# Kernel tuning notes

Measured on AMD Instinct MI355X. Metric: run time of the kernel, lower is better.

Reference implementation:

```python
import jax, jax.numpy as jnp
import numpy as np

DIM = 1024
H = 8            # heads (light and heavy)
DH = 64          # dim_head
W = 64           # local attention window (light_window_size // 2)
NQ = 512         # num_heavy_tokens_q
NKV = 1024       # num_heavy_tokens_kv
EPS = 1.0        # coor descent eps
NITERS = 50      # coor descent iters
FETCH = 9.0 / 8.0
SCALE = DH ** -0.5


def _ln(x, w, b):
    m = x.mean(-1, keepdims=True)
    v = ((x - m) ** 2).mean(-1, keepdims=True)
    return (x - m) * jax.lax.rsqrt(v + 1e-5) * w + b


def _rms(x, g):
    n = jnp.maximum(jnp.linalg.norm(x, axis=-1, keepdims=True), 1e-12)
    return x / n * np.sqrt(DIM).astype(np.float32) * g


def local_attn(x, Wqkv, Wout):
    # LocalMHA, non-causal, look_backward=1, look_forward=1, window W
    b, n, _ = x.shape
    nw = n // W
    qkv = x @ Wqkv.T                      # [b,n,3*H*DH]
    q, k, v = jnp.split(qkv, 3, axis=-1)
    def towin(t):
        return t.reshape(b, nw, W, H, DH).transpose(0, 3, 1, 2, 4)  # [b,h,nw,w,dh]
    q, k, v = map(towin, (q, k, v))
    def expand(t):  # gather prev/cur/next windows -> [b,h,nw,3w,dh]
        tp = jnp.pad(t, ((0, 0), (0, 0), (1, 1), (0, 0), (0, 0)))
        return jnp.concatenate([tp[:, :, :-2], tp[:, :, 1:-1], tp[:, :, 2:]], axis=3)
    ke, ve = expand(k), expand(v)
    sim = jnp.einsum('bhnid,bhnjd->bhnij', q, ke) * SCALE
    win = jnp.arange(nw)
    valid = jnp.concatenate([
        jnp.repeat((win > 0)[:, None], W, 1),
        jnp.ones((nw, W), bool),
        jnp.repeat((win < nw - 1)[:, None], W, 1)], axis=1)  # [nw,3w]
    sim = jnp.where(valid[None, None, :, None, :], sim, -1e9)
    attn = jax.nn.softmax(sim, axis=-1)
    o = jnp.einsum('bhnij,bhnjd->bhnid', attn, ve)
    o = o.transpose(0, 2, 3, 1, 4).reshape(b, n, H * DH)
    return o @ Wout.T


def route(x, routing_token, num_tokens):
    # CoordinateDescentRouter with num_routing_tokens=1, straight_through=True
    s = jnp.einsum('bnd,rd->brn', x, routing_token).reshape(x.shape[0], x.shape[1])
    n = s.shape[-1]
    logk = jnp.log(jnp.asarray(min(num_tokens * FETCH, float(n)), s.dtype))
    def body(ab, _):
        a, bb = ab
        a = EPS * (logk - jax.nn.logsumexp((s + bb) / EPS, axis=-1, keepdims=True))
        bb = -jax.nn.relu(s + a)
        return (a, bb), None
    (a, bb), _ = jax.lax.scan(body, (jnp.zeros((s.shape[0], 1), s.dtype), -s), None, length=NITERS)
    scores = jnp.exp((s + a + bb) / EPS)
    sel_scores, sel_idx = jax.lax.top_k(scores, num_tokens)
    # straight-through: forward value 1.0, gradient of identity
    sel_scores = sel_scores + jax.lax.stop_gradient(1.0 - sel_scores)
    return sel_scores, sel_idx


def heavy_attn(xq, ctx, scores_kv, gamma, Wq, Wkv, Wout, null_kv):
    b = xq.shape[0]
    xq = _rms(xq, gamma)
    ctx = _rms(ctx, gamma)
    q = (xq @ Wq.T).reshape(b, -1, H, DH).transpose(0, 2, 1, 3)           # [b,h,nq,dh]
    kv = (ctx @ Wkv.T).reshape(b, -1, H, 2 * DH).transpose(0, 2, 1, 3)    # [b,h,nkv,2dh]
    k, v = kv[..., :DH], kv[..., DH:]
    v = v * scores_kv[:, None, :, None]
    nk = jnp.broadcast_to(null_kv[0][None, :, None, :], (b, H, 1, DH))
    nv = jnp.broadcast_to(null_kv[1][None, :, None, :], (b, H, 1, DH))
    k = jnp.concatenate([nk, k], axis=2)
    v = jnp.concatenate([nv, v], axis=2)
    sim = jnp.einsum('bhid,bhjd->bhij', q, k) * SCALE
    attn = jax.nn.softmax(sim, axis=-1)
    o = jnp.einsum('bhij,bhjd->bhid', attn, v)
    o = o.transpose(0, 2, 1, 3).reshape(b, -1, H * DH)
    return o @ Wout.T


def setup_inputs() -> dict:
    key = jax.random.key(0)
    ks = jax.random.split(key, 12)
    D, IN = DIM, H * DH
    w = lambda k, shape: jax.random.normal(k, shape, jnp.float32) * 0.02
    return {
        'x': jax.random.normal(ks[0], (4, 4096, D), jnp.float32),
        'ln_w': jnp.ones((D,), jnp.float32),
        'ln_b': jnp.zeros((D,), jnp.float32),
        'Wqkv': w(ks[1], (3 * IN, D)),
        'Wout_l': w(ks[2], (D, IN)),
        'rt_q': jax.random.normal(ks[3], (1, D), jnp.float32),
        'rt_kv': jax.random.normal(ks[4], (1, D), jnp.float32),
        'gamma': jnp.ones((D,), jnp.float32),
        'Wq': w(ks[5], (IN, D)),
        'Wkv': w(ks[6], (2 * IN, D)),
        'Wout_h': w(ks[7], (D, IN)),
        'null_kv': jax.random.normal(ks[8], (2, H, DH), jnp.float32),
        'null_q': jax.random.normal(ks[9], (D,), jnp.float32),
    }


def reference(x, ln_w, ln_b, Wqkv, Wout_l, rt_q, rt_kv, gamma, Wq, Wkv, Wout_h, null_kv, null_q):
    b, n, d = x.shape
    light = local_attn(_ln(x, ln_w, ln_b), Wqkv, Wout_l)
    sq, iq = route(x, rt_q, NQ)
    skv, ikv = route(x, rt_kv, NKV)
    br = jnp.arange(b)[:, None]
    xq = x[br, iq]          # gather routed queries  [b,NQ,d]
    xkv = x[br, ikv]        # gather routed kv       [b,NKV,d]
    heavy = heavy_attn(xq, xkv, skv, gamma, Wq, Wkv, Wout_h, null_kv)
    heavy = heavy * sq[..., None]
    out = jnp.broadcast_to(null_q[None, None, :], (b, n, d))
    out = out.at[br, iq].set(heavy)   # scatter heavy branch back
    return out + light
```

## Files before the change

kernel.cpp:

```cpp
#include <hip/hip_runtime.h>
#include <hip/hip_bf16.h>

typedef __attribute__((ext_vector_type(8))) short bv8;
typedef __attribute__((ext_vector_type(4))) float fv4;
typedef __hip_bfloat16 bf16;

#define MFMA16(a,b,c) __builtin_amdgcn_mfma_f32_16x16x32_bf16((a),(b),(c),0,0,0)
#define GLOAD_LDS(gp, lp) __builtin_amdgcn_global_load_lds( \
    (const __attribute__((address_space(1))) void*)(gp), \
    (__attribute__((address_space(3))) void*)(lp), 16, 0, 0)

template<int NW>
__device__ __forceinline__ float blockReduceSumF(float v) {
  #pragma unroll
  for (int m = 1; m < 64; m <<= 1) v += __shfl_xor(v, m, 64);
  __shared__ float sm[NW];
  if ((threadIdx.x & 63) == 0) sm[threadIdx.x >> 6] = v;
  __syncthreads();
  float t = 0.f;
  #pragma unroll
  for (int i = 0; i < NW; ++i) t += sm[i];
  __syncthreads();
  return t;
}

template<int NW>
__device__ __forceinline__ double blockReduceMaxD(double v) {
  #pragma unroll
  for (int m = 1; m < 64; m <<= 1) v = fmax(v, __shfl_xor(v, m, 64));
  __shared__ double sm[NW];
  if ((threadIdx.x & 63) == 0) sm[threadIdx.x >> 6] = v;
  __syncthreads();
  double t = sm[0];
  #pragma unroll
  for (int i = 1; i < NW; ++i) t = fmax(t, sm[i]);
  __syncthreads();
  return t;
}

__global__ __launch_bounds__(256)
void cast5_kernel(const float* __restrict__ a0, const float* __restrict__ a1,
                  const float* __restrict__ a2, const float* __restrict__ a3,
                  const float* __restrict__ a4,
                  bf16* __restrict__ b0, bf16* __restrict__ b1, bf16* __restrict__ b2,
                  bf16* __restrict__ b3, bf16* __restrict__ b4) {
  size_t g = ((size_t)blockIdx.x * 256 + threadIdx.x) * 8;
  const float* src; bf16* dst; size_t off;
  if (g < 1572864)      { src = a0; dst = b0; off = g; }
  else if (g < 2097152) { src = a1; dst = b1; off = g - 1572864; }
  else if (g < 2621440) { src = a2; dst = b2; off = g - 2097152; }
  else if (g < 3670016) { src = a3; dst = b3; off = g - 2621440; }
  else                  { src = a4; dst = b4; off = g - 3670016; }
  float4 v0 = *(const float4*)(src + off);
  float4 v1 = *(const float4*)(src + off + 4);
  bv8 o;
  ((bf16*)&o)[0] = __float2bfloat16(v0.x); ((bf16*)&o)[1] = __float2bfloat16(v0.y);
  ((bf16*)&o)[2] = __float2bfloat16(v0.z); ((bf16*)&o)[3] = __float2bfloat16(v0.w);
  ((bf16*)&o)[4] = __float2bfloat16(v1.x); ((bf16*)&o)[5] = __float2bfloat16(v1.y);
  ((bf16*)&o)[6] = __float2bfloat16(v1.z); ((bf16*)&o)[7] = __float2bfloat16(v1.w);
  *(bv8*)(dst + off) = o;
}

__global__ __launch_bounds__(256)
void ln_sdot_kernel(const float* __restrict__ x, const float* __restrict__ w,
                    const float* __restrict__ bb, const float* __restrict__ rtq,
                    const float* __restrict__ rtkv, bf16* __restrict__ out,
                    double* __restrict__ s) {
  const int r = blockIdx.x;
  const float* xr = x + (size_t)r * 1024;
  float v4[4]; float ssum = 0.f;
  double dq = 0.0, dk = 0.0;
  #pragma unroll
  for (int i = 0; i < 4; ++i) {
    int d = threadIdx.x + i * 256;
    float v = xr[d];
    v4[i] = v; ssum += v;
    dq += (double)v * (double)rtq[d];
    dk += (double)v * (double)rtkv[d];
  }
  ssum = blockReduceSumF<4>(ssum);
  const float mean = ssum * (1.0f / 1024.0f);
  float vs = 0.f;
  #pragma unroll
  for (int i = 0; i < 4; ++i) { float d = v4[i] - mean; vs += d * d; }
  vs = blockReduceSumF<4>(vs);
  const float rstd = 1.0f / sqrtf(vs * (1.0f / 1024.0f) + 1e-5f);
  #pragma unroll
  for (int m = 1; m < 64; m <<= 1) { dq += __shfl_xor(dq, m, 64); dk += __shfl_xor(dk, m, 64); }
  __shared__ double smq[4], smk[4];
  if ((threadIdx.x & 63) == 0) { smq[threadIdx.x >> 6] = dq; smk[threadIdx.x >> 6] = dk; }
  __syncthreads();
  if (threadIdx.x == 0) {
    s[r] = smq[0] + smq[1] + smq[2] + smq[3];
    s[16384 + r] = smk[0] + smk[1] + smk[2] + smk[3];
  }
  bf16* orow = out + (size_t)r * 1024;
  #pragma unroll
  for (int i = 0; i < 4; ++i) {
    int d = threadIdx.x + i * 256;
    orow[d] = __float2bfloat16((v4[i] - mean) * rstd * w[d] + bb[d]);
  }
}

__global__ __launch_bounds__(256, 1)
void route_sel_kernel(const double* __restrict__ s_all, int* __restrict__ iq,
                      int* __restrict__ ikv, int* __restrict__ posq) {
  const int route = blockIdx.x >> 2, b = blockIdx.x & 3;
  const double* s = s_all + route * 16384 + b * 4096;
  const double K = (route == 0) ? 576.0 : 1152.0;
  const int KSEL = (route == 0) ? 512 : 1024;
  const int tid = threadIdx.x;
  const int lane = tid & 63, wid = tid >> 6;
  __shared__ double evbuf[4096];
  __shared__ double a_sh;
  __shared__ int scn[256];

  double sv[16];
  #pragma unroll
  for (int i = 0; i < 16; ++i) sv[i] = s[tid * 16 + i];
  double mx = sv[0];
  #pragma unroll
  for (int i = 1; i < 16; ++i) mx = fmax(mx, sv[i]);
  mx = blockReduceMaxD<4>(mx);
  #pragma unroll
  for (int i = 0; i < 16; ++i) evbuf[tid * 16 + i] = exp(sv[i] - mx);
  __syncthreads();

  if (wid == 0) {
    double e64[64];
    #pragma unroll
    for (int j = 0; j < 64; ++j) e64[j] = evbuf[j * 64 + lane];
    double z = (4096.0 / K) * exp(-mx);
    for (int it = 1; it < 50; ++it) {
      double a0 = 0.0, a1 = 0.0, a2 = 0.0, a3 = 0.0;
      #pragma unroll
      for (int j = 0; j < 64; j += 4) {
        a0 += fmin(e64[j], z);
        a1 += fmin(e64[j + 1], z);
        a2 += fmin(e64[j + 2], z);
        a3 += fmin(e64[j + 3], z);
      }
      double t = (a0 + a1) + (a2 + a3);
      #pragma unroll
      for (int m = 1; m < 64; m <<= 1) t += __shfl_xor(t, m, 64);
      z = t / K;
    }
    if (lane == 0) a_sh = -mx - log(z);
  }
  __syncthreads();
  const double a = a_sh;

  float scf[16]; int m16 = 0;
  #pragma unroll
  for (int i = 0; i < 16; ++i) {
    scf[i] = (float)exp(fmin(sv[i] + a, 0.0));
    m16 += (scf[i] == 1.0f) ? 1 : 0;
  }
  scn[tid] = m16;
  __syncthreads();
  for (int off = 1; off < 256; off <<= 1) {
    int v = (tid >= off) ? scn[tid - off] : 0;
    __syncthreads();
    scn[tid] += v;
    __syncthreads();
  }
  const int total = scn[255];
  const int excl = scn[tid] - m16;
  if (total >= KSEL) {
    int rk = excl;
    #pragma unroll
    for (int i = 0; i < 16; ++i) {
      if (scf[i] == 1.0f) {
        if (rk < KSEL) {
          int idx = tid * 16 + i;
          if (route == 0) { iq[b * 512 + rk] = idx; posq[b * 4096 + idx] = rk; }
          else            { ikv[b * 1024 + rk] = idx; }
        }
        rk++;
      }
    }
  } else {
    unsigned long long* keys = (unsigned long long*)evbuf;
    #pragma unroll
    for (int i = 0; i < 16; ++i) {
      unsigned bits = __float_as_uint(scf[i]);
      keys[tid * 16 + i] = ((unsigned long long)(~bits) << 32) | (unsigned long long)(tid * 16 + i);
    }
    for (int k = 2; k <= 4096; k <<= 1) {
      for (int j = k >> 1; j > 0; j >>= 1) {
        __syncthreads();
        for (int t = tid; t < 2048; t += 256) {
          int i2 = ((t & ~(j - 1)) << 1) | (t & (j - 1));
          int ip = i2 + j;
          unsigned long long av = keys[i2], bvv = keys[ip];
          bool up = ((i2 & k) == 0);
          if (up ? (av > bvv) : (av < bvv)) { keys[i2] = bvv; keys[ip] = av; }
        }
      }
    }
    __syncthreads();
    for (int j2 = tid; j2 < KSEL; j2 += 256) {
      int idx = (int)(keys[j2] & 0xFFFFFFFFull);
      if (route == 0) { iq[b * 512 + j2] = idx; posq[b * 4096 + idx] = j2; }
      else            { ikv[b * 1024 + j2] = idx; }
    }
  }
}

__global__ __launch_bounds__(256)
void gather_rms_kernel(const float* __restrict__ x, const float* __restrict__ gamma,
                       const int* __restrict__ iq, const int* __restrict__ ikv,
                       bf16* __restrict__ xq, bf16* __restrict__ xkv) {
  const int bid = blockIdx.x;
  const float* src; bf16* dst;
  if (bid < 2048) {
    int b = bid >> 9, j = bid & 511;
    int tok = iq[b * 512 + j];
    src = x + ((size_t)(b * 4096 + tok)) * 1024;
    dst = xq + (size_t)bid * 1024;
  } else {
    int id = bid - 2048;
    int b = id >> 10, j = id & 1023;
    int tok = ikv[b * 1024 + j];
    src = x + ((size_t)(b * 4096 + tok)) * 1024;
    dst = xkv + (size_t)id * 1024;
  }
  float v4[4]; float ss = 0.f;
  #pragma unroll
  for (int i = 0; i < 4; ++i) { v4[i] = src[threadIdx.x + i * 256]; ss += v4[i] * v4[i]; }
  ss = blockReduceSumF<4>(ss);
  const float nrm = fmaxf(sqrtf(ss), 1e-12f);
  const float scl = 32.0f / nrm;
  #pragma unroll
  for (int i = 0; i < 4; ++i) {
    int d = threadIdx.x + i * 256;
    dst[d] = __float2bfloat16(v4[i] * scl * gamma[d]);
  }
}

template<int EPI>
__global__ __launch_bounds__(256)
void gemm_bt(const bf16* __restrict__ A, const bf16* __restrict__ B, void* __restrict__ Cout,
             int M, int N, int K,
             const int* __restrict__ posq, const float* __restrict__ heavy,
             const float* __restrict__ nullq) {
  __shared__ alignas(16) bf16 As[128 * 32];
  __shared__ alignas(16) bf16 Bs[128 * 32];
  const int tid = threadIdx.x;
  const int lane = tid & 63, w = tid >> 6;
  const int wr = w >> 1, wc = w & 1;
  const int lrow = lane & 15, lk = (lane >> 4) * 8;
  const int d = blockIdx.y * gridDim.x + blockIdx.x;
  const int q = d >> 3;
  const int col = q % gridDim.x;
  const int panel = (d & 7) + 8 * (q / gridDim.x);
  const int row0 = panel * 128, col0 = col * 128;
  fv4 acc[4][4];
  #pragma unroll
  for (int m = 0; m < 4; ++m)
    #pragma unroll
    for (int n = 0; n < 4; ++n) acc[m][n] = (fv4){0.f, 0.f, 0.f, 0.f};
  const int ob0 = w * 2048;
  for (int k0 = 0; k0 < K; k0 += 32) {
    #pragma unroll
    for (int t = 0; t < 2; ++t) {
      int ob = ob0 + t * 1024;
      int ofl = ob + lane * 16;
      int r = ofl >> 6, c8 = ((ofl >> 4) & 3) * 8;
      GLOAD_LDS(A + (size_t)(row0 + r) * K + k0 + c8, (char*)As + ob);
      GLOAD_LDS(B + (size_t)(col0 + r) * K + k0 + c8, (char*)Bs + ob);
    }
    __syncthreads();
    bv8 af[4], bfr[4];
    #pragma unroll
    for (int m = 0; m < 4; ++m) af[m] = *(bv8*)&As[(wr * 64 + m * 16 + lrow) * 32 + lk];
    #pragma unroll
    for (int n = 0; n < 4; ++n) bfr[n] = *(bv8*)&Bs[(wc * 64 + n * 16 + lrow) * 32 + lk];
    #pragma unroll
    for (int m = 0; m < 4; ++m)
      #pragma unroll
      for (int n = 0; n < 4; ++n)
        acc[m][n] = MFMA16(af[m], bfr[n], acc[m][n]);
    __syncthreads();
  }
  #pragma unroll
  for (int m = 0; m < 4; ++m) {
    int gr0 = row0 + wr * 64 + m * 16 + (lane >> 4) * 4;
    #pragma unroll
    for (int n = 0; n < 4; ++n) {
      int gc = col0 + wc * 64 + n * 16 + lrow;
      #pragma unroll
      for (int r = 0; r < 4; ++r) {
        int grow = gr0 + r;
        float vv = acc[m][n][r];
        if (EPI == 0) {
          ((bf16*)Cout)[(size_t)grow * N + gc] = __float2bfloat16(vv);
        } else if (EPI == 1) {
          ((float*)Cout)[(size_t)grow * N + gc] = vv;
        } else {
          int p = posq[grow];
          float add = (p >= 0) ? heavy[((size_t)((grow >> 12) * 512 + p)) * 1024 + gc]
                               : nullq[gc];
          ((float*)Cout)[(size_t)grow * N + gc] = vv + add;
        }
      }
    }
  }
}

__global__ __launch_bounds__(256)
void local_attn_kernel(const bf16* __restrict__ qkv, bf16* __restrict__ olight) {
  const int w = blockIdx.x, h = blockIdx.y, b = blockIdx.z;
  const int tid = threadIdx.x;
  const int lane = tid & 63, wv = tid >> 6;
  const int lrow = lane & 15, lkg = lane >> 4;
  __shared__ bf16 Qs[64][72], Ks[64][72], Vts[64][72], Ps[64][72];
  {
    const size_t baseq = ((size_t)(b * 4096 + w * 64)) * 1536 + h * 64;
    #pragma unroll
    for (int v = 0; v < 2; ++v) {
      int vec = tid + v * 256; int i = vec >> 3, dd = (vec & 7) * 8;
      *(bv8*)&Qs[i][dd] = *(const bv8*)&qkv[baseq + (size_t)i * 1536 + dd];
    }
  }
  fv4 oacc[4];
  float m_run[4], l_run[4];
  #pragma unroll
  for (int n = 0; n < 4; ++n) oacc[n] = (fv4){0.f, 0.f, 0.f, 0.f};
  #pragma unroll
  for (int r = 0; r < 4; ++r) { m_run[r] = -INFINITY; l_run[r] = 0.f; }
  for (int c = 0; c < 3; ++c) {
    int sw = w - 1 + c;
    if (sw < 0 || sw >= 64) continue;
    __syncthreads();
    const size_t bkv = ((size_t)(b * 4096 + sw * 64)) * 1536 + h * 64;
    #pragma unroll
    for (int v = 0; v < 2; ++v) {
      int vec = tid + v * 256; int i = vec >> 3, dd = (vec & 7) * 8;
      *(bv8*)&Ks[i][dd] = *(const bv8*)&qkv[bkv + 512 + (size_t)i * 1536 + dd];
    }
    #pragma unroll
    for (int v = 0; v < 2; ++v) {
      int vec = tid + v * 256; int j = vec >> 3, d0 = (vec & 7) * 8;
      bv8 val = *(const bv8*)&qkv[bkv + 1024 + (size_t)j * 1536 + d0];
      #pragma unroll
      for (int i = 0; i < 8; ++i) Vts[d0 + i][j] = ((bf16*)&val)[i];
    }
    __syncthreads();
    fv4 sa[4];
    #pragma unroll
    for (int n = 0; n < 4; ++n) {
      sa[n] = (fv4){0.f, 0.f, 0.f, 0.f};
      #pragma unroll
      for (int ks = 0; ks < 2; ++ks) {
        bv8 aq = *(bv8*)&Qs[wv * 16 + lrow][lkg * 8 + ks * 32];
        bv8 bk = *(bv8*)&Ks[n * 16 + lrow][lkg * 8 + ks * 32];
        sa[n] = MFMA16(aq, bk, sa[n]);
      }
    }
    float mc[4];
    #pragma unroll
    for (int r = 0; r < 4; ++r) {
      #pragma unroll
      for (int n = 0; n < 4; ++n) sa[n][r] *= 0.125f;
      mc[r] = fmaxf(fmaxf(sa[0][r], sa[1][r]), fmaxf(sa[2][r], sa[3][r]));
    }
    #pragma unroll
    for (int m = 1; m < 16; m <<= 1)
      #pragma unroll
      for (int r = 0; r < 4; ++r) mc[r] = fmaxf(mc[r], __shfl_xor(mc[r], m, 64));
    float p[4][4], ls[4];
    #pragma unroll
    for (int r = 0; r < 4; ++r) {
      float mn = fmaxf(m_run[r], mc[r]);
      float scl = expf(m_run[r] - mn);
      ls[r] = 0.f;
      #pragma unroll
      for (int n = 0; n < 4; ++n) { p[n][r] = expf(sa[n][r] - mn); ls[r] += p[n][r]; }
      m_run[r] = mn;
      l_run[r] *= scl;
      #pragma unroll
      for (int n = 0; n < 4; ++n) oacc[n][r] *= scl;
    }
    #pragma unroll
    for (int m = 1; m < 16; m <<= 1)
      #pragma unroll
      for (int r = 0; r < 4; ++r) ls[r] += __shfl_xor(ls[r], m, 64);
    #pragma unroll
    for (int r = 0; r < 4; ++r) l_run[r] += ls[r];
    #pragma unroll
    for (int n = 0; n < 4; ++n)
      #pragma unroll
      for (int r = 0; r < 4; ++r)
        Ps[wv * 16 + lkg * 4 + r][n * 16 + lrow] = __float2bfloat16(p[n][r]);
    __syncthreads();
    #pragma unroll
    for (int n = 0; n < 4; ++n)
      #pragma unroll
      for (int ks = 0; ks < 2; ++ks) {
        bv8 ap = *(bv8*)&Ps[wv * 16 + lrow][lkg * 8 + ks * 32];
        bv8 bvv = *(bv8*)&Vts[n * 16 + lrow][lkg * 8 + ks * 32];
        oacc[n] = MFMA16(ap, bvv, oacc[n]);
      }
  }
  const size_t ob = ((size_t)(b * 4096 + w * 64 + wv * 16)) * 512 + h * 64;
  #pragma unroll
  for (int n = 0; n < 4; ++n)
    #pragma unroll
    for (int r = 0; r < 4; ++r) {
      int row = lkg * 4 + r;
      olight[ob + (size_t)row * 512 + n * 16 + lrow] = __float2bfloat16(oacc[n][r] / l_run[r]);
    }
}

__global__ __launch_bounds__(256)
void heavy_attn_split_kernel(const bf16* __restrict__ qh, const bf16* __restrict__ kvh,
                             const float* __restrict__ nkv, float* __restrict__ o_part,
                             float* __restrict__ ml_part) {
  const int qt = blockIdx.x, h = blockIdx.y;
  const int b = blockIdx.z >> 2, s = blockIdx.z & 3;
  const int tid = threadIdx.x;
  const int lane = tid & 63, wv = tid >> 6;
  const int lrow = lane & 15, lkg = lane >> 4;
  __shared__ bf16 Qs[64][72], Ks[64][72], Vts[64][72], Ps[64][72];
  {
    const size_t baseq = ((size_t)(b * 512 + qt * 64)) * 512 + h * 64;
    #pragma unroll
    for (int v = 0; v < 2; ++v) {
      int vec = tid + v * 256; int i = vec >> 3, dd = (vec & 7) * 8;
      *(bv8*)&Qs[i][dd] = *(const bv8*)&qh[baseq + (size_t)i * 512 + dd];
    }
  }
  fv4 oacc[4];
  float m_run[4], l_run[4];
  #pragma unroll
  for (int n = 0; n < 4; ++n) oacc[n] = (fv4){0.f, 0.f, 0.f, 0.f};
  #pragma unroll
  for (int r = 0; r < 4; ++r) { m_run[r] = -INFINITY; l_run[r] = 0.f; }
  const int cs = (s == 0) ? 0 : (s * 4 + 1);
  const int ce = s * 4 + 5;
  for (int c = cs; c < ce; ++c) {
    __syncthreads();
    #pragma unroll
    for (int v = 0; v < 2; ++v) {
      int vec = tid + v * 256; int j = vec >> 3, dd = (vec & 7) * 8;
      int kvg = c * 64 + j;
      bv8 val;
      if (kvg >= 1 && kvg <= 1024) {
        val = *(const bv8*)&kvh[((size_t)(b * 1024 + kvg - 1)) * 1024 + h * 128 + dd];
      } else if (kvg == 0) {
        #pragma unroll
        for (int t = 0; t < 8; ++t) ((bf16*)&val)[t] = __float2bfloat16(nkv[h * 64 + dd + t]);
      } else {
        #pragma unroll
        for (int t = 0; t < 8; ++t) ((short*)&val)[t] = 0;
      }
      *(bv8*)&Ks[j][dd] = val;
    }
    #pragma unroll
    for (int v = 0; v < 2; ++v) {
      int vec = tid + v * 256; int j = vec >> 3, d0 = (vec & 7) * 8;
      int kvg = c * 64 + j;
      if (kvg >= 1 && kvg <= 1024) {
        bv8 val = *(const bv8*)&kvh[((size_t)(b * 1024 + kvg - 1)) * 1024 + h * 128 + 64 + d0];
        #pragma unroll
        for (int i = 0; i < 8; ++i) Vts[d0 + i][j] = ((bf16*)&val)[i];
      } else if (kvg == 0) {
        #pragma unroll
        for (int i = 0; i < 8; ++i) Vts[d0 + i][j] = __float2bfloat16(nkv[512 + h * 64 + d0 + i]);
      } else {
        #pragma unroll
        for (int i = 0; i < 8; ++i) Vts[d0 + i][j] = __float2bfloat16(0.0f);
      }
    }
    __syncthreads();
    fv4 sa[4];
    #pragma unroll
    for (int n = 0; n < 4; ++n) {
      sa[n] = (fv4){0.f, 0.f, 0.f, 0.f};
      #pragma unroll
      for (int ks = 0; ks < 2; ++ks) {
        bv8 aq = *(bv8*)&Qs[wv * 16 + lrow][lkg * 8 + ks * 32];
        bv8 bk = *(bv8*)&Ks[n * 16 + lrow][lkg * 8 + ks * 32];
        sa[n] = MFMA16(aq, bk, sa[n]);
      }
    }
    float mc[4];
    #pragma unroll
    for (int r = 0; r < 4; ++r) {
      #pragma unroll
      for (int n = 0; n < 4; ++n) {
        sa[n][r] *= 0.125f;
        int kvg = c * 64 + n * 16 + lrow;
        if (kvg > 1024) sa[n][r] = -1e30f;
      }
      mc[r] = fmaxf(fmaxf(sa[0][r], sa[1][r]), fmaxf(sa[2][r], sa[3][r]));
    }
    #pragma unroll
    for (int m = 1; m < 16; m <<= 1)
      #pragma unroll
      for (int r = 0; r < 4; ++r) mc[r] = fmaxf(mc[r], __shfl_xor(mc[r], m, 64));
    float p[4][4], ls[4];
    #pragma unroll
    for (int r = 0; r < 4; ++r) {
      float mn = fmaxf(m_run[r], mc[r]);
      float scl = expf(m_run[r] - mn);
      ls[r] = 0.f;
      #pragma unroll
      for (int n = 0; n < 4; ++n) { p[n][r] = expf(sa[n][r] - mn); ls[r] += p[n][r]; }
      m_run[r] = mn;
      l_run[r] *= scl;
      #pragma unroll
      for (int n = 0; n < 4; ++n) oacc[n][r] *= scl;
    }
    #pragma unroll
    for (int m = 1; m < 16; m <<= 1)
      #pragma unroll
      for (int r = 0; r < 4; ++r) ls[r] += __shfl_xor(ls[r], m, 64);
    #pragma unroll
    for (int r = 0; r < 4; ++r) l_run[r] += ls[r];
    #pragma unroll
    for (int n = 0; n < 4; ++n)
      #pragma unroll
      for (int r = 0; r < 4; ++r)
        Ps[wv * 16 + lkg * 4 + r][n * 16 + lrow] = __float2bfloat16(p[n][r]);
    __syncthreads();
    #pragma unroll
    for (int n = 0; n < 4; ++n)
      #pragma unroll
      for (int ks = 0; ks < 2; ++ks) {
        bv8 ap = *(bv8*)&Ps[wv * 16 + lrow][lkg * 8 + ks * 32];
        bv8 bvv = *(bv8*)&Vts[n * 16 + lrow][lkg * 8 + ks * 32];
        oacc[n] = MFMA16(ap, bvv, oacc[n]);
      }
  }
  const int idx = (((s * 4 + b) * 8 + h) * 8 + qt);
  float* ob = o_part + (size_t)idx * 4096;
  #pragma unroll
  for (int n = 0; n < 4; ++n)
    #pragma unroll
    for (int r = 0; r < 4; ++r) {
      int row = wv * 16 + lkg * 4 + r;
      ob[row * 64 + n * 16 + lrow] = oacc[n][r];
    }
  if (lrow == 0) {
    #pragma unroll
    for (int r = 0; r < 4; ++r) {
      int row = wv * 16 + lkg * 4 + r;
      ml_part[idx * 128 + row] = m_run[r];
      ml_part[idx * 128 + 64 + row] = l_run[r];
    }
  }
}

__global__ __launch_bounds__(256)
void heavy_combine_kernel(const float* __restrict__ o_part, const float* __restrict__ ml_part,
                          bf16* __restrict__ oh) {
  const int qt = blockIdx.x, h = blockIdx.y, b = blockIdx.z;
  const int tid = threadIdx.x;
  const int row = tid >> 2, c0 = (tid & 3) * 16;
  int idx[4]; float m[4], l[4];
  #pragma unroll
  for (int s = 0; s < 4; ++s) {
    idx[s] = (((s * 4 + b) * 8 + h) * 8 + qt);
    m[s] = ml_part[idx[s] * 128 + row];
    l[s] = ml_part[idx[s] * 128 + 64 + row];
  }
  const float mstar = fmaxf(fmaxf(m[0], m[1]), fmaxf(m[2], m[3]));
  float wsum = 0.f, w[4];
  #pragma unroll
  for (int s = 0; s < 4; ++s) { w[s] = expf(m[s] - mstar); wsum += w[s] * l[s]; }
  const float inv = 1.0f / wsum;
  float o[16];
  #pragma unroll
  for (int i = 0; i < 16; ++i) o[i] = 0.f;
  #pragma unroll
  for (int s = 0; s < 4; ++s) {
    const fv4* op = (const fv4*)(o_part + (size_t)idx[s] * 4096 + row * 64 + c0);
    #pragma unroll
    for (int k = 0; k < 4; ++k) {
      fv4 v = op[k];
      #pragma unroll
      for (int j = 0; j < 4; ++j) o[k * 4 + j] += w[s] * v[j];
    }
  }
  const size_t ob = ((size_t)(b * 512 + qt * 64 + row)) * 512 + h * 64 + c0;
  bv8 pk[2];
  #pragma unroll
  for (int i = 0; i < 16; ++i) ((bf16*)pk)[i] = __float2bfloat16(o[i] * inv);
  *(bv8*)&oh[ob] = pk[0];
  *(bv8*)&oh[ob + 8] = pk[1];
}

extern "C" void kernel_launch(void* const* d_in, const int* in_sizes, int n_in,
                              void* d_out, int out_size, void* d_ws, size_t ws_size,
                              hipStream_t stream) {
  (void)in_sizes; (void)n_in; (void)out_size; (void)ws_size;
  const float* x     = (const float*)d_in[0];
  const float* ln_w  = (const float*)d_in[1];
  const float* ln_b  = (const float*)d_in[2];
  const float* Wqkv  = (const float*)d_in[3];
  const float* Woutl = (const float*)d_in[4];
  const float* rtq   = (const float*)d_in[5];
  const float* rtkv  = (const float*)d_in[6];
  const float* gamma = (const float*)d_in[7];
  const float* Wq    = (const float*)d_in[8];
  const float* Wkv   = (const float*)d_in[9];
  const float* Wouth = (const float*)d_in[10];
  const float* nkv   = (const float*)d_in[11];
  const float* nq    = (const float*)d_in[12];
  float* out = (float*)d_out;

  char* ws = (char*)d_ws;
  size_t off = 0;
  auto alloc = [&](size_t bytes) -> void* {
    void* p = ws + off;
    off = (off + bytes + 255) & ~(size_t)255;
    return p;
  };
  bf16* ln_bf    = (bf16*)alloc(16384ull * 1024 * 2);
  bf16* qkv_bf   = (bf16*)alloc(16384ull * 1536 * 2);
  bf16* ol_bf    = (bf16*)alloc(16384ull * 512 * 2);
  bf16* Wqkv_bf  = (bf16*)alloc(1536ull * 1024 * 2);
  bf16* Woutl_bf = (bf16*)alloc(1024ull * 512 * 2);
  bf16* Wq_bf    = (bf16*)alloc(512ull * 1024 * 2);
  bf16* Wkv_bf   = (bf16*)alloc(1024ull * 1024 * 2);
  bf16* Wouth_bf = (bf16*)alloc(1024ull * 512 * 2);
  double* s_d    = (double*)alloc(32768ull * 8);
  int* iq        = (int*)alloc(2048ull * 4);
  int* ikv       = (int*)alloc(4096ull * 4);
  int* posq      = (int*)alloc(16384ull * 4);
  bf16* xq_bf    = (bf16*)alloc(2048ull * 1024 * 2);
  bf16* xkv_bf   = (bf16*)alloc(4096ull * 1024 * 2);
  bf16* qh_bf    = (bf16*)alloc(2048ull * 512 * 2);
  bf16* kvh_bf   = (bf16*)alloc(4096ull * 1024 * 2);
  bf16* oh_bf    = (bf16*)alloc(2048ull * 512 * 2);
  float* heavy_f = (float*)alloc(2048ull * 1024 * 4);
  float* o_part  = (float*)alloc(4096ull * 4096 * 4);
  float* ml_part = (float*)alloc(4096ull * 128 * 4);

  cast5_kernel<<<2048, 256, 0, stream>>>(Wqkv, Woutl, Wq, Wkv, Wouth,
                                         Wqkv_bf, Woutl_bf, Wq_bf, Wkv_bf, Wouth_bf);

  ln_sdot_kernel<<<16384, 256, 0, stream>>>(x, ln_w, ln_b, rtq, rtkv, ln_bf, s_d);

  hipMemsetAsync(posq, 0xFF, 16384 * 4, stream);
  route_sel_kernel<<<8, 256, 0, stream>>>(s_d, iq, ikv, posq);

  gemm_bt<0><<<dim3(12, 128), 256, 0, stream>>>(ln_bf, Wqkv_bf, qkv_bf, 16384, 1536, 1024,
                                                nullptr, nullptr, nullptr);
  local_attn_kernel<<<dim3(64, 8, 4), 256, 0, stream>>>(qkv_bf, ol_bf);

  gather_rms_kernel<<<6144, 256, 0, stream>>>(x, gamma, iq, ikv, xq_bf, xkv_bf);
  gemm_bt<0><<<dim3(4, 16), 256, 0, stream>>>(xq_bf, Wq_bf, qh_bf, 2048, 512, 1024,
                                              nullptr, nullptr, nullptr);
  gemm_bt<0><<<dim3(8, 32), 256, 0, stream>>>(xkv_bf, Wkv_bf, kvh_bf, 4096, 1024, 1024,
                                              nullptr, nullptr, nullptr);
  heavy_attn_split_kernel<<<dim3(8, 8, 16), 256, 0, stream>>>(qh_bf, kvh_bf, nkv, o_part, ml_part);
  heavy_combine_kernel<<<dim3(8, 8, 4), 256, 0, stream>>>(o_part, ml_part, oh_bf);
  gemm_bt<1><<<dim3(8, 16), 256, 0, stream>>>(oh_bf, Wouth_bf, heavy_f, 2048, 1024, 512,
                                              nullptr, nullptr, nullptr);

  gemm_bt<2><<<dim3(8, 128), 256, 0, stream>>>(ol_bf, Woutl_bf, out, 16384, 1024, 512,
                                               posq, heavy_f, nq);
}
```

Measured before the change: 326.7 us.

## Merge independent kernels into combined launches and store split partials in bf16

Several launches are merged into single kernels that branch on block index. The weight cast, LayerNorm/routing-dot and posq memset become one prep kernel. Local attention and the routed gather+RMSNorm share one launch, and the Wq and Wkv projection GEMMs share another, which cuts launch gaps and lets small kernels fill the GPU together. Split-KV heavy attention partial outputs are also stored as bf16 instead of fp32, halving that traffic at some cost in precision.

```diff
diff --git a/kernel.cpp b/kernel.cpp
--- a/kernel.cpp
+++ b/kernel.cpp
@@ -39,66 +39,71 @@
 }
 
 __global__ __launch_bounds__(256)
-void cast5_kernel(const float* __restrict__ a0, const float* __restrict__ a1,
-                  const float* __restrict__ a2, const float* __restrict__ a3,
-                  const float* __restrict__ a4,
-                  bf16* __restrict__ b0, bf16* __restrict__ b1, bf16* __restrict__ b2,
-                  bf16* __restrict__ b3, bf16* __restrict__ b4) {
-  size_t g = ((size_t)blockIdx.x * 256 + threadIdx.x) * 8;
-  const float* src; bf16* dst; size_t off;
-  if (g < 1572864)      { src = a0; dst = b0; off = g; }
-  else if (g < 2097152) { src = a1; dst = b1; off = g - 1572864; }
-  else if (g < 2621440) { src = a2; dst = b2; off = g - 2097152; }
-  else if (g < 3670016) { src = a3; dst = b3; off = g - 2621440; }
-  else                  { src = a4; dst = b4; off = g - 3670016; }
-  float4 v0 = *(const float4*)(src + off);
-  float4 v1 = *(const float4*)(src + off + 4);
-  bv8 o;
-  ((bf16*)&o)[0] = __float2bfloat16(v0.x); ((bf16*)&o)[1] = __float2bfloat16(v0.y);
-  ((bf16*)&o)[2] = __float2bfloat16(v0.z); ((bf16*)&o)[3] = __float2bfloat16(v0.w);
-  ((bf16*)&o)[4] = __float2bfloat16(v1.x); ((bf16*)&o)[5] = __float2bfloat16(v1.y);
-  ((bf16*)&o)[6] = __float2bfloat16(v1.z); ((bf16*)&o)[7] = __float2bfloat16(v1.w);
-  *(bv8*)(dst + off) = o;
-}
-
-__global__ __launch_bounds__(256)
-void ln_sdot_kernel(const float* __restrict__ x, const float* __restrict__ w,
-                    const float* __restrict__ bb, const float* __restrict__ rtq,
-                    const float* __restrict__ rtkv, bf16* __restrict__ out,
-                    double* __restrict__ s) {
-  const int r = blockIdx.x;
-  const float* xr = x + (size_t)r * 1024;
-  float v4[4]; float ssum = 0.f;
-  double dq = 0.0, dk = 0.0;
-  #pragma unroll
-  for (int i = 0; i < 4; ++i) {
-    int d = threadIdx.x + i * 256;
-    float v = xr[d];
-    v4[i] = v; ssum += v;
-    dq += (double)v * (double)rtq[d];
-    dk += (double)v * (double)rtkv[d];
-  }
-  ssum = blockReduceSumF<4>(ssum);
-  const float mean = ssum * (1.0f / 1024.0f);
-  float vs = 0.f;
-  #pragma unroll
-  for (int i = 0; i < 4; ++i) { float d = v4[i] - mean; vs += d * d; }
-  vs = blockReduceSumF<4>(vs);
-  const float rstd = 1.0f / sqrtf(vs * (1.0f / 1024.0f) + 1e-5f);
-  #pragma unroll
-  for (int m = 1; m < 64; m <<= 1) { dq += __shfl_xor(dq, m, 64); dk += __shfl_xor(dk, m, 64); }
-  __shared__ double smq[4], smk[4];
-  if ((threadIdx.x & 63) == 0) { smq[threadIdx.x >> 6] = dq; smk[threadIdx.x >> 6] = dk; }
-  __syncthreads();
-  if (threadIdx.x == 0) {
-    s[r] = smq[0] + smq[1] + smq[2] + smq[3];
-    s[16384 + r] = smk[0] + smk[1] + smk[2] + smk[3];
-  }
-  bf16* orow = out + (size_t)r * 1024;
-  #pragma unroll
-  for (int i = 0; i < 4; ++i) {
-    int d = threadIdx.x + i * 256;
-    orow[d] = __float2bfloat16((v4[i] - mean) * rstd * w[d] + bb[d]);
+void prep_kernel(const float* __restrict__ x, const float* __restrict__ lnw,
+                 const float* __restrict__ lnb, const float* __restrict__ rtq,
+                 const float* __restrict__ rtkv, bf16* __restrict__ lnout,
+                 double* __restrict__ s,
+                 const float* __restrict__ a0, const float* __restrict__ a1,
+                 const float* __restrict__ a2, const float* __restrict__ a3,
+                 const float* __restrict__ a4,
+                 bf16* __restrict__ b0, bf16* __restrict__ b1, bf16* __restrict__ b2,
+                 bf16* __restrict__ b3, bf16* __restrict__ b4,
+                 int* __restrict__ posq) {
+  const int bid = blockIdx.x;
+  if (bid < 16384) {
+    const int r = bid;
+    const float* xr = x + (size_t)r * 1024;
+    float v4[4]; float ssum = 0.f;
+    double dq = 0.0, dk = 0.0;
+    #pragma unroll
+    for (int i = 0; i < 4; ++i) {
+      int d = threadIdx.x + i * 256;
+      float v = xr[d];
+      v4[i] = v; ssum += v;
+      dq += (double)v * (double)rtq[d];
+      dk += (double)v * (double)rtkv[d];
+    }
+    ssum = blockReduceSumF<4>(ssum);
+    const float mean = ssum * (1.0f / 1024.0f);
+    float vs = 0.f;
+    #pragma unroll
+    for (int i = 0; i < 4; ++i) { float d = v4[i] - mean; vs += d * d; }
+    vs = blockReduceSumF<4>(vs);
+    const float rstd = 1.0f / sqrtf(vs * (1.0f / 1024.0f) + 1e-5f);
+    #pragma unroll
+    for (int m = 1; m < 64; m <<= 1) { dq += __shfl_xor(dq, m, 64); dk += __shfl_xor(dk, m, 64); }
+    __shared__ double smq[4], smk[4];
+    if ((threadIdx.x & 63) == 0) { smq[threadIdx.x >> 6] = dq; smk[threadIdx.x >> 6] = dk; }
+    __syncthreads();
+    if (threadIdx.x == 0) {
+      s[r] = smq[0] + smq[1] + smq[2] + smq[3];
+      s[16384 + r] = smk[0] + smk[1] + smk[2] + smk[3];
+    }
+    bf16* orow = lnout + (size_t)r * 1024;
+    #pragma unroll
+    for (int i = 0; i < 4; ++i) {
+      int d = threadIdx.x + i * 256;
+      orow[d] = __float2bfloat16((v4[i] - mean) * rstd * lnw[d] + lnb[d]);
+    }
+  } else if (bid < 18432) {
+    size_t g = ((size_t)(bid - 16384) * 256 + threadIdx.x) * 8;
+    const float* src; bf16* dst; size_t off;
+    if (g < 1572864)      { src = a0; dst = b0; off = g; }
+    else if (g < 2097152) { src = a1; dst = b1; off = g - 1572864; }
+    else if (g < 2621440) { src = a2; dst = b2; off = g - 2097152; }
+    else if (g < 3670016) { src = a3; dst = b3; off = g - 2621440; }
+    else                  { src = a4; dst = b4; off = g - 3670016; }
+    float4 v0 = *(const float4*)(src + off);
+    float4 v1 = *(const float4*)(src + off + 4);
+    bv8 o;
+    ((bf16*)&o)[0] = __float2bfloat16(v0.x); ((bf16*)&o)[1] = __float2bfloat16(v0.y);
+    ((bf16*)&o)[2] = __float2bfloat16(v0.z); ((bf16*)&o)[3] = __float2bfloat16(v0.w);
+    ((bf16*)&o)[4] = __float2bfloat16(v1.x); ((bf16*)&o)[5] = __float2bfloat16(v1.y);
+    ((bf16*)&o)[6] = __float2bfloat16(v1.z); ((bf16*)&o)[7] = __float2bfloat16(v1.w);
+    *(bv8*)(dst + off) = o;
+  } else {
+    int i0 = (bid - 18432) * 1024 + threadIdx.x * 4;
+    posq[i0] = -1; posq[i0 + 1] = -1; posq[i0 + 2] = -1; posq[i0 + 3] = -1;
   }
 }
 
@@ -207,54 +212,16 @@
   }
 }
 
-__global__ __launch_bounds__(256)
-void gather_rms_kernel(const float* __restrict__ x, const float* __restrict__ gamma,
-                       const int* __restrict__ iq, const int* __restrict__ ikv,
-                       bf16* __restrict__ xq, bf16* __restrict__ xkv) {
-  const int bid = blockIdx.x;
-  const float* src; bf16* dst;
-  if (bid < 2048) {
-    int b = bid >> 9, j = bid & 511;
-    int tok = iq[b * 512 + j];
-    src = x + ((size_t)(b * 4096 + tok)) * 1024;
-    dst = xq + (size_t)bid * 1024;
-  } else {
-    int id = bid - 2048;
-    int b = id >> 10, j = id & 1023;
-    int tok = ikv[b * 1024 + j];
-    src = x + ((size_t)(b * 4096 + tok)) * 1024;
-    dst = xkv + (size_t)id * 1024;
-  }
-  float v4[4]; float ss = 0.f;
-  #pragma unroll
-  for (int i = 0; i < 4; ++i) { v4[i] = src[threadIdx.x + i * 256]; ss += v4[i] * v4[i]; }
-  ss = blockReduceSumF<4>(ss);
-  const float nrm = fmaxf(sqrtf(ss), 1e-12f);
-  const float scl = 32.0f / nrm;
-  #pragma unroll
-  for (int i = 0; i < 4; ++i) {
-    int d = threadIdx.x + i * 256;
-    dst[d] = __float2bfloat16(v4[i] * scl * gamma[d]);
-  }
-}
-
 template<int EPI>
-__global__ __launch_bounds__(256)
-void gemm_bt(const bf16* __restrict__ A, const bf16* __restrict__ B, void* __restrict__ Cout,
-             int M, int N, int K,
-             const int* __restrict__ posq, const float* __restrict__ heavy,
-             const float* __restrict__ nullq) {
-  __shared__ alignas(16) bf16 As[128 * 32];
-  __shared__ alignas(16) bf16 Bs[128 * 32];
+__device__ __forceinline__ void gemm_core(
+    const bf16* __restrict__ A, const bf16* __restrict__ B, void* __restrict__ Cout,
+    int N, int K, int row0, int col0, bf16* As, bf16* Bs,
+    const int* __restrict__ posq, const float* __restrict__ heavy,
+    const float* __restrict__ nullq) {
   const int tid = threadIdx.x;
   const int lane = tid & 63, w = tid >> 6;
   const int wr = w >> 1, wc = w & 1;
   const int lrow = lane & 15, lk = (lane >> 4) * 8;
-  const int d = blockIdx.y * gridDim.x + blockIdx.x;
-  const int q = d >> 3;
-  const int col = q % gridDim.x;
-  const int panel = (d & 7) + 8 * (q / gridDim.x);
-  const int row0 = panel * 128, col0 = col * 128;
   fv4 acc[4][4];
   #pragma unroll
   for (int m = 0; m < 4; ++m)
@@ -308,114 +275,182 @@
   }
 }
 
+__device__ __forceinline__ void xcd_remap(int d, int gx, int& row0, int& col0) {
+  int q = d >> 3;
+  col0 = (q % gx) * 128;
+  row0 = ((d & 7) + 8 * (q / gx)) * 128;
+}
+
+template<int EPI>
 __global__ __launch_bounds__(256)
-void local_attn_kernel(const bf16* __restrict__ qkv, bf16* __restrict__ olight) {
-  const int w = blockIdx.x, h = blockIdx.y, b = blockIdx.z;
+void gemm_bt(const bf16* __restrict__ A, const bf16* __restrict__ B, void* __restrict__ Cout,
+             int N, int K,
+             const int* __restrict__ posq, const float* __restrict__ heavy,
+             const float* __restrict__ nullq) {
+  __shared__ alignas(16) bf16 As[128 * 32];
+  __shared__ alignas(16) bf16 Bs[128 * 32];
+  int row0, col0;
+  xcd_remap(blockIdx.y * gridDim.x + blockIdx.x, gridDim.x, row0, col0);
+  gemm_core<EPI>(A, B, Cout, N, K, row0, col0, As, Bs, posq, heavy, nullq);
+}
+
+__global__ __launch_bounds__(256)
+void wqkv_gemm_kernel(const bf16* __restrict__ xkv, const bf16* __restrict__ Wkv,
+                      bf16* __restrict__ kvh,
+                      const bf16* __restrict__ xq, const bf16* __restrict__ Wq,
+                      bf16* __restrict__ qh) {
+  __shared__ alignas(16) bf16 As[128 * 32];
+  __shared__ alignas(16) bf16 Bs[128 * 32];
+  const int bid = blockIdx.x;
+  int row0, col0;
+  if (bid < 256) {
+    xcd_remap(bid, 8, row0, col0);
+    gemm_core<0>(xkv, Wkv, kvh, 1024, 1024, row0, col0, As, Bs, nullptr, nullptr, nullptr);
+  } else {
+    xcd_remap(bid - 256, 4, row0, col0);
+    gemm_core<0>(xq, Wq, qh, 512, 1024, row0, col0, As, Bs, nullptr, nullptr, nullptr);
+  }
+}
+
+__global__ __launch_bounds__(256)
+void la_gather_kernel(const bf16* __restrict__ qkv, bf16* __restrict__ olight,
+                      const float* __restrict__ x, const float* __restrict__ gamma,
+                      const int* __restrict__ iq, const int* __restrict__ ikv,
+                      bf16* __restrict__ xq, bf16* __restrict__ xkv) {
+  __shared__ bf16 Qs[64][72], Ks[64][72], Vts[64][72], Ps[64][72];
   const int tid = threadIdx.x;
-  const int lane = tid & 63, wv = tid >> 6;
-  const int lrow = lane & 15, lkg = lane >> 4;
-  __shared__ bf16 Qs[64][72], Ks[64][72], Vts[64][72], Ps[64][72];
-  {
-    const size_t baseq = ((size_t)(b * 4096 + w * 64)) * 1536 + h * 64;
-    #pragma unroll
-    for (int v = 0; v < 2; ++v) {
-      int vec = tid + v * 256; int i = vec >> 3, dd = (vec & 7) * 8;
-      *(bv8*)&Qs[i][dd] = *(const bv8*)&qkv[baseq + (size_t)i * 1536 + dd];
-    }
-  }
-  fv4 oacc[4];
-  float m_run[4], l_run[4];
-  #pragma unroll
-  for (int n = 0; n < 4; ++n) oacc[n] = (fv4){0.f, 0.f, 0.f, 0.f};
-  #pragma unroll
-  for (int r = 0; r < 4; ++r) { m_run[r] = -INFINITY; l_run[r] = 0.f; }
-  for (int c = 0; c < 3; ++c) {
-    int sw = w - 1 + c;
-    if (sw < 0 || sw >= 64) continue;
-    __syncthreads();
-    const size_t bkv = ((size_t)(b * 4096 + sw * 64)) * 1536 + h * 64;
-    #pragma unroll
-    for (int v = 0; v < 2; ++v) {
-      int vec = tid + v * 256; int i = vec >> 3, dd = (vec & 7) * 8;
-      *(bv8*)&Ks[i][dd] = *(const bv8*)&qkv[bkv + 512 + (size_t)i * 1536 + dd];
-    }
-    #pragma unroll
-    for (int v = 0; v < 2; ++v) {
-      int vec = tid + v * 256; int j = vec >> 3, d0 = (vec & 7) * 8;
-      bv8 val = *(const bv8*)&qkv[bkv + 1024 + (size_t)j * 1536 + d0];
-      #pragma unroll
-      for (int i = 0; i < 8; ++i) Vts[d0 + i][j] = ((bf16*)&val)[i];
-    }
-    __syncthreads();
-    fv4 sa[4];
-    #pragma unroll
-    for (int n = 0; n < 4; ++n) {
-      sa[n] = (fv4){0.f, 0.f, 0.f, 0.f};
-      #pragma unroll
-      for (int ks = 0; ks < 2; ++ks) {
-        bv8 aq = *(bv8*)&Qs[wv * 16 + lrow][lkg * 8 + ks * 32];
-        bv8 bk = *(bv8*)&Ks[n * 16 + lrow][lkg * 8 + ks * 32];
-        sa[n] = MFMA16(aq, bk, sa[n]);
-      }
-    }
-    float mc[4];
-    #pragma unroll
-    for (int r = 0; r < 4; ++r) {
-      #pragma unroll
-      for (int n = 0; n < 4; ++n) sa[n][r] *= 0.125f;
-      mc[r] = fmaxf(fmaxf(sa[0][r], sa[1][r]), fmaxf(sa[2][r], sa[3][r]));
-    }
-    #pragma unroll
-    for (int m = 1; m < 16; m <<= 1)
-      #pragma unroll
-      for (int r = 0; r < 4; ++r) mc[r] = fmaxf(mc[r], __shfl_xor(mc[r], m, 64));
-    float p[4][4], ls[4];
-    #pragma unroll
-    for (int r = 0; r < 4; ++r) {
-      float mn = fmaxf(m_run[r], mc[r]);
-      float scl = expf(m_run[r] - mn);
-      ls[r] = 0.f;
-      #pragma unroll
-      for (int n = 0; n < 4; ++n) { p[n][r] = expf(sa[n][r] - mn); ls[r] += p[n][r]; }
-      m_run[r] = mn;
-      l_run[r] *= scl;
-      #pragma unroll
-      for (int n = 0; n < 4; ++n) oacc[n][r] *= scl;
-    }
-    #pragma unroll
-    for (int m = 1; m < 16; m <<= 1)
-      #pragma unroll
-      for (int r = 0; r < 4; ++r) ls[r] += __shfl_xor(ls[r], m, 64);
-    #pragma unroll
-    for (int r = 0; r < 4; ++r) l_run[r] += ls[r];
+  if (blockIdx.x < 2048) {
+    const int w = blockIdx.x & 63, h = (blockIdx.x >> 6) & 7, b = blockIdx.x >> 9;
+    const int lane = tid & 63, wv = tid >> 6;
+    const int lrow = lane & 15, lkg = lane >> 4;
+    {
+      const size_t baseq = ((size_t)(b * 4096 + w * 64)) * 1536 + h * 64;
+      #pragma unroll
+      for (int v = 0; v < 2; ++v) {
+        int vec = tid + v * 256; int i = vec >> 3, dd = (vec & 7) * 8;
+        *(bv8*)&Qs[i][dd] = *(const bv8*)&qkv[baseq + (size_t)i * 1536 + dd];
+      }
+    }
+    fv4 oacc[4];
+    float m_run[4], l_run[4];
+    #pragma unroll
+    for (int n = 0; n < 4; ++n) oacc[n] = (fv4){0.f, 0.f, 0.f, 0.f};
+    #pragma unroll
+    for (int r = 0; r < 4; ++r) { m_run[r] = -INFINITY; l_run[r] = 0.f; }
+    for (int c = 0; c < 3; ++c) {
+      int sw = w - 1 + c;
+      if (sw < 0 || sw >= 64) continue;
+      __syncthreads();
+      const size_t bkv = ((size_t)(b * 4096 + sw * 64)) * 1536 + h * 64;
+      #pragma unroll
+      for (int v = 0; v < 2; ++v) {
+        int vec = tid + v * 256; int i = vec >> 3, dd = (vec & 7) * 8;
+        *(bv8*)&Ks[i][dd] = *(const bv8*)&qkv[bkv + 512 + (size_t)i * 1536 + dd];
+      }
+      #pragma unroll
+      for (int v = 0; v < 2; ++v) {
+        int vec = tid + v * 256; int j = vec >> 3, d0 = (vec & 7) * 8;
+        bv8 val = *(const bv8*)&qkv[bkv + 1024 + (size_t)j * 1536 + d0];
+        #pragma unroll
+        for (int i = 0; i < 8; ++i) Vts[d0 + i][j] = ((bf16*)&val)[i];
+      }
+      __syncthreads();
+      fv4 sa[4];
+      #pragma unroll
+      for (int n = 0; n < 4; ++n) {
+        sa[n] = (fv4){0.f, 0.f, 0.f, 0.f};
+        #pragma unroll
+        for (int ks = 0; ks < 2; ++ks) {
+          bv8 aq = *(bv8*)&Qs[wv * 16 + lrow][lkg * 8 + ks * 32];
+          bv8 bk = *(bv8*)&Ks[n * 16 + lrow][lkg * 8 + ks * 32];
+          sa[n] = MFMA16(aq, bk, sa[n]);
+        }
+      }
+      float mc[4];
+      #pragma unroll
+      for (int r = 0; r < 4; ++r) {
+        #pragma unroll
+        for (int n = 0; n < 4; ++n) sa[n][r] *= 0.125f;
+        mc[r] = fmaxf(fmaxf(sa[0][r], sa[1][r]), fmaxf(sa[2][r], sa[3][r]));
+      }
+      #pragma unroll
+      for (int m = 1; m < 16; m <<= 1)
+        #pragma unroll
+        for (int r = 0; r < 4; ++r) mc[r] = fmaxf(mc[r], __shfl_xor(mc[r], m, 64));
+      float p[4][4], ls[4];
+      #pragma unroll
+      for (int r = 0; r < 4; ++r) {
+        float mn = fmaxf(m_run[r], mc[r]);
+        float scl = expf(m_run[r] - mn);
+        ls[r] = 0.f;
+        #pragma unroll
+        for (int n = 0; n < 4; ++n) { p[n][r] = expf(sa[n][r] - mn); ls[r] += p[n][r]; }
+        m_run[r] = mn;
+        l_run[r] *= scl;
+        #pragma unroll
+        for (int n = 0; n < 4; ++n) oacc[n][r] *= scl;
+      }
+      #pragma unroll
+      for (int m = 1; m < 16; m <<= 1)
+        #pragma unroll
+        for (int r = 0; r < 4; ++r) ls[r] += __shfl_xor(ls[r], m, 64);
+      #pragma unroll
+      for (int r = 0; r < 4; ++r) l_run[r] += ls[r];
+      #pragma unroll
+      for (int n = 0; n < 4; ++n)
+        #pragma unroll
+        for (int r = 0; r < 4; ++r)
+          Ps[wv * 16 + lkg * 4 + r][n * 16 + lrow] = __float2bfloat16(p[n][r]);
+      __syncthreads();
+      #pragma unroll
+      for (int n = 0; n < 4; ++n)
+        #pragma unroll
+        for (int ks = 0; ks < 2; ++ks) {
+          bv8 ap = *(bv8*)&Ps[wv * 16 + lrow][lkg * 8 + ks * 32];
+          bv8 bvv = *(bv8*)&Vts[n * 16 + lrow][lkg * 8 + ks * 32];
+          oacc[n] = MFMA16(ap, bvv, oacc[n]);
+        }
+    }
+    const size_t ob = ((size_t)(b * 4096 + w * 64 + wv * 16)) * 512 + h * 64;
     #pragma unroll
     for (int n = 0; n < 4; ++n)
       #pragma unroll
-      for (int r = 0; r < 4; ++r)
-        Ps[wv * 16 + lkg * 4 + r][n * 16 + lrow] = __float2bfloat16(p[n][r]);
-    __syncthreads();
-    #pragma unroll
-    for (int n = 0; n < 4; ++n)
-      #pragma unroll
-      for (int ks = 0; ks < 2; ++ks) {
-        bv8 ap = *(bv8*)&Ps[wv * 16 + lrow][lkg * 8 + ks * 32];
-        bv8 bvv = *(bv8*)&Vts[n * 16 + lrow][lkg * 8 + ks * 32];
-        oacc[n] = MFMA16(ap, bvv, oacc[n]);
-      }
-  }
-  const size_t ob = ((size_t)(b * 4096 + w * 64 + wv * 16)) * 512 + h * 64;
-  #pragma unroll
-  for (int n = 0; n < 4; ++n)
-    #pragma unroll
-    for (int r = 0; r < 4; ++r) {
-      int row = lkg * 4 + r;
-      olight[ob + (size_t)row * 512 + n * 16 + lrow] = __float2bfloat16(oacc[n][r] / l_run[r]);
-    }
+      for (int r = 0; r < 4; ++r) {
+        int row = lkg * 4 + r;
+        olight[ob + (size_t)row * 512 + n * 16 + lrow] = __float2bfloat16(oacc[n][r] / l_run[r]);
+      }
+  } else {
+    const int bid = blockIdx.x - 2048;
+    const float* src; bf16* dst;
+    if (bid < 2048) {
+      int b = bid >> 9, j = bid & 511;
+      int tok = iq[b * 512 + j];
+      src = x + ((size_t)(b * 4096 + tok)) * 1024;
+      dst = xq + (size_t)bid * 1024;
+    } else {
+      int id = bid - 2048;
+      int b = id >> 10, j = id & 1023;
+      int tok = ikv[b * 1024 + j];
+      src = x + ((size_t)(b * 4096 + tok)) * 1024;
+      dst = xkv + (size_t)id * 1024;
+    }
+    float v4[4]; float ss = 0.f;
+    #pragma unroll
+    for (int i = 0; i < 4; ++i) { v4[i] = src[tid + i * 256]; ss += v4[i] * v4[i]; }
+    ss = blockReduceSumF<4>(ss);
+    const float nrm = fmaxf(sqrtf(ss), 1e-12f);
+    const float scl = 32.0f / nrm;
+    #pragma unroll
+    for (int i = 0; i < 4; ++i) {
+      int d = tid + i * 256;
+      dst[d] = __float2bfloat16(v4[i] * scl * gamma[d]);
+    }
+  }
 }
 
 __global__ __launch_bounds__(256)
 void heavy_attn_split_kernel(const bf16* __restrict__ qh, const bf16* __restrict__ kvh,
-                             const float* __restrict__ nkv, float* __restrict__ o_part,
+                             const float* __restrict__ nkv, bf16* __restrict__ o_part,
                              float* __restrict__ ml_part) {
   const int qt = blockIdx.x, h = blockIdx.y;
   const int b = blockIdx.z >> 2, s = blockIdx.z & 3;
@@ -535,13 +570,13 @@
       }
   }
   const int idx = (((s * 4 + b) * 8 + h) * 8 + qt);
-  float* ob = o_part + (size_t)idx * 4096;
+  bf16* ob = o_part + (size_t)idx * 4096;
   #pragma unroll
   for (int n = 0; n < 4; ++n)
     #pragma unroll
     for (int r = 0; r < 4; ++r) {
       int row = wv * 16 + lkg * 4 + r;
-      ob[row * 64 + n * 16 + lrow] = oacc[n][r];
+      ob[row * 64 + n * 16 + lrow] = __float2bfloat16(oacc[n][r]);
     }
   if (lrow == 0) {
     #pragma unroll
@@ -554,7 +589,7 @@
 }
 
 __global__ __launch_bounds__(256)
-void heavy_combine_kernel(const float* __restrict__ o_part, const float* __restrict__ ml_part,
+void heavy_combine_kernel(const bf16* __restrict__ o_part, const float* __restrict__ ml_part,
                           bf16* __restrict__ oh) {
   const int qt = blockIdx.x, h = blockIdx.y, b = blockIdx.z;
   const int tid = threadIdx.x;
@@ -576,13 +611,13 @@
   for (int i = 0; i < 16; ++i) o[i] = 0.f;
   #pragma unroll
   for (int s = 0; s < 4; ++s) {
-    const fv4* op = (const fv4*)(o_part + (size_t)idx[s] * 4096 + row * 64 + c0);
-    #pragma unroll
-    for (int k = 0; k < 4; ++k) {
-      fv4 v = op[k];
-      #pragma unroll
-      for (int j = 0; j < 4; ++j) o[k * 4 + j] += w[s] * v[j];
-    }
+    const bf16* op = o_part + (size_t)idx[s] * 4096 + row * 64 + c0;
+    bv8 v0 = *(const bv8*)op;
+    bv8 v1 = *(const bv8*)(op + 8);
+    #pragma unroll
+    for (int j = 0; j < 8; ++j) o[j] += w[s] * __bfloat162float(((bf16*)&v0)[j]);
+    #pragma unroll
+    for (int j = 0; j < 8; ++j) o[8 + j] += w[s] * __bfloat162float(((bf16*)&v1)[j]);
   }
   const size_t ob = ((size_t)(b * 512 + qt * 64 + row)) * 512 + h * 64 + c0;
   bv8 pk[2];
@@ -636,31 +671,28 @@
   bf16* kvh_bf   = (bf16*)alloc(4096ull * 1024 * 2);
   bf16* oh_bf    = (bf16*)alloc(2048ull * 512 * 2);
   float* heavy_f = (float*)alloc(2048ull * 1024 * 4);
-  float* o_part  = (float*)alloc(4096ull * 4096 * 4);
+  bf16* o_part   = (bf16*)alloc(4096ull * 4096 * 2);
   float* ml_part = (float*)alloc(4096ull * 128 * 4);
 
-  cast5_kernel<<<2048, 256, 0, stream>>>(Wqkv, Woutl, Wq, Wkv, Wouth,
-                                         Wqkv_bf, Woutl_bf, Wq_bf, Wkv_bf, Wouth_bf);
-
-  ln_sdot_kernel<<<16384, 256, 0, stream>>>(x, ln_w, ln_b, rtq, rtkv, ln_bf, s_d);
-
-  hipMemsetAsync(posq, 0xFF, 16384 * 4, stream);
+  prep_kernel<<<18448, 256, 0, stream>>>(x, ln_w, ln_b, rtq, rtkv, ln_bf, s_d,
+                                         Wqkv, Woutl, Wq, Wkv, Wouth,
+                                         Wqkv_bf, Woutl_bf, Wq_bf, Wkv_bf, Wouth_bf,
+                                         posq);
+
   route_sel_kernel<<<8, 256, 0, stream>>>(s_d, iq, ikv, posq);
 
-  gemm_bt<0><<<dim3(12, 128), 256, 0, stream>>>(ln_bf, Wqkv_bf, qkv_bf, 16384, 1536, 1024,
+  gemm_bt<0><<<dim3(12, 128), 256, 0, stream>>>(ln_bf, Wqkv_bf, qkv_bf, 1536, 1024,
                                                 nullptr, nullptr, nullptr);
-  local_attn_kernel<<<dim3(64, 8, 4), 256, 0, stream>>>(qkv_bf, ol_bf);
-
-  gather_rms_kernel<<<6144, 256, 0, stream>>>(x, gamma, iq, ikv, xq_bf, xkv_bf);
-  gemm_bt<0><<<dim3(4, 16), 256, 0, stream>>>(xq_bf, Wq_bf, qh_bf, 2048, 512, 1024,
-                                              nullptr, nullptr, nullptr);
-  gemm_bt<0><<<dim3(8, 32), 256, 0, stream>>>(xkv_bf, Wkv_bf, kvh_bf, 4096, 1024, 1024,
-                                              nullptr, nullptr, nullptr);
+
+  la_gather_kernel<<<8192, 256, 0, stream>>>(qkv_bf, ol_bf, x, gamma, iq, ikv, xq_bf, xkv_bf);
+
+  wqkv_gemm_kernel<<<320, 256, 0, stream>>>(xkv_bf, Wkv_bf, kvh_bf, xq_bf, Wq_bf, qh_bf);
+
   heavy_attn_split_kernel<<<dim3(8, 8, 16), 256, 0, stream>>>(qh_bf, kvh_bf, nkv, o_part, ml_part);
   heavy_combine_kernel<<<dim3(8, 8, 4), 256, 0, stream>>>(o_part, ml_part, oh_bf);
-  gemm_bt<1><<<dim3(8, 16), 256, 0, stream>>>(oh_bf, Wouth_bf, heavy_f, 2048, 1024, 512,
+  gemm_bt<1><<<dim3(8, 16), 256, 0, stream>>>(oh_bf, Wouth_bf, heavy_f, 1024, 512,
                                               nullptr, nullptr, nullptr);
 
-  gemm_bt<2><<<dim3(8, 128), 256, 0, stream>>>(ol_bf, Woutl_bf, out, 16384, 1024, 512,
+  gemm_bt<2><<<dim3(8, 128), 256, 0, stream>>>(ol_bf, Woutl_bf, out, 1024, 512,
                                                posq, heavy_f, nq);
 }
```

Result: faster. 293.7 us (-10.1%).
